# Kernel tuning notes

Hardware: AMD Instinct MI355X
Metric: run time of the kernel (lower is better)

## Reference

```python
import jax, jax.numpy as jnp
import numpy as np

ENS, S_DIM, A_DIM, R_DIM, HID, LAYER_NUM = 7, 30, 8, 1, 200, 5
N_HID_LAYERS = LAYER_NUM - 2  # hidden->hidden Linear+Swish blocks


def swish(x):
    return x * jax.nn.sigmoid(x)


def setup_inputs() -> dict:
    key = jax.random.key(0)
    ks = jax.random.split(key, 14)
    N = 32768
    out_dim = S_DIM + R_DIM
    s = jax.random.normal(ks[0], (N, ENS, S_DIM), dtype=jnp.float32)
    a = jax.random.normal(ks[1], (N, ENS, A_DIM), dtype=jnp.float32)
    sc = 0.05
    W1 = jax.random.normal(ks[2], (ENS, S_DIM + A_DIM, HID), dtype=jnp.float32) * sc
    b1 = jax.random.normal(ks[3], (ENS, HID), dtype=jnp.float32) * sc
    Wh = jax.random.normal(ks[4], (N_HID_LAYERS, ENS, HID, HID), dtype=jnp.float32) * sc
    bh = jax.random.normal(ks[5], (N_HID_LAYERS, ENS, HID), dtype=jnp.float32) * sc
    Wmu = jax.random.normal(ks[6], (ENS, HID, out_dim), dtype=jnp.float32) * sc
    bmu = jax.random.normal(ks[7], (ENS, out_dim), dtype=jnp.float32) * sc
    Wsig = jax.random.normal(ks[8], (ENS, HID, out_dim), dtype=jnp.float32) * sc
    bsig = jax.random.normal(ks[9], (ENS, out_dim), dtype=jnp.float32) * sc
    max_lv_s = jnp.ones((1, S_DIM), dtype=jnp.float32) / 2.0
    min_lv_s = jnp.ones((1, S_DIM), dtype=jnp.float32) * -10.0
    max_lv_r = jnp.ones((1, R_DIM), dtype=jnp.float32) / 2.0
    min_lv_r = jnp.ones((1, R_DIM), dtype=jnp.float32) * -10.0
    return {"s": s, "a": a, "W1": W1, "b1": b1, "Wh": Wh, "bh": bh,
            "Wmu": Wmu, "bmu": bmu, "Wsig": Wsig, "bsig": bsig,
            "max_lv_s": max_lv_s, "min_lv_s": min_lv_s,
            "max_lv_r": max_lv_r, "min_lv_r": min_lv_r}


def reference(s, a, W1, b1, Wh, bh, Wmu, bmu, Wsig, bsig,
              max_lv_s, min_lv_s, max_lv_r, min_lv_r):
    # x: [N, E, s+a]; per-ensemble-member weights batched along E
    x = jnp.concatenate([s, a], axis=-1)
    h = swish(jnp.einsum('ned,edh->neh', x, W1) + b1)
    for i in range(Wh.shape[0]):
        h = swish(jnp.einsum('neh,ehk->nek', h, Wh[i]) + bh[i])
    mu = jnp.einsum('neh,eho->neo', h, Wmu) + bmu      # [N, E, s+r]
    sigma = jnp.einsum('neh,eho->neo', h, Wsig) + bsig  # raw logvar/2
    ds_mu, r_mu = mu[..., :S_DIM], mu[..., S_DIM:]
    ds_sg, r_sg = sigma[..., :S_DIM], sigma[..., S_DIM:]
    # soft clamping of log-variance, then exp
    ds_sg = (max_lv_s - jax.nn.softplus(max_lv_s - 2.0 * ds_sg)) / 2.0
    ds_sg = (min_lv_s + jax.nn.softplus(2.0 * ds_sg - min_lv_s)) / 2.0
    ds_sg = jnp.exp(ds_sg)
    r_sg = (max_lv_r - jax.nn.softplus(max_lv_r - 2.0 * r_sg)) / 2.0
    r_sg = (min_lv_r + jax.nn.softplus(2.0 * r_sg - min_lv_r)) / 2.0
    r_sg = jnp.exp(r_sg)
    return ((ds_mu, ds_sg), (r_mu, r_sg))
```

## Files before the change

kernel.cpp:

```cpp
#include <hip/hip_runtime.h>
#include <hip/hip_bf16.h>

#define ENS 7
#define SDIM 30
#define ADIM 8
#define DIN 38
#define HID 200
#define DOUT 31
#define NHL 3
#define HS 232
#define MT 64

typedef __bf16 bf16x8 __attribute__((ext_vector_type(8)));
typedef float f32x4 __attribute__((ext_vector_type(4)));

#define U_L1 13312
#define U_H 46592
#define OFF_HD2 (U_L1 + NHL * U_H)
#define PER_E (OFF_HD2 + 14336)
#define WS_TOTAL (ENS * PER_E)

__device__ __forceinline__ unsigned short f2bf(float f) {
    unsigned u = __float_as_uint(f);
    u += 0x7fffu + ((u >> 16) & 1u);
    return (unsigned short)(u >> 16);
}

__device__ __forceinline__ unsigned pk2(float a, float b) {
    __hip_bfloat162 h = __float22bfloat162_rn(make_float2(a, b));
    return *reinterpret_cast<unsigned*>(&h);
}

__device__ __forceinline__ float softplusf(float x) {
    return fmaxf(x, 0.f) + __logf(1.f + __expf(-fabsf(x)));
}

__global__ void prep_kernel(const float* __restrict__ W1, const float* __restrict__ Wh,
                            const float* __restrict__ Wmu, const float* __restrict__ Wsig,
                            unsigned short* __restrict__ ws) {
    int idx = blockIdx.x * 256 + threadIdx.x;
    if (idx >= WS_TOTAL) return;
    int e = idx / PER_E, r = idx % PER_E;
    int j = r & 7, lane = (r >> 3) & 63;
    int l16 = lane & 15, q = lane >> 4;
    float v = 0.f;
    if (r < U_L1) {
        int fi = r >> 9;
        int ct = fi >> 1, st = fi & 1;
        int k = st * 32 + q * 8 + j, n = ct * 16 + l16;
        if (k < DIN && n < HID) v = W1[(e * DIN + k) * HID + n];
    } else if (r < OFF_HD2) {
        int rh = r - U_L1;
        int l = rh / U_H, r2 = rh % U_H;
        int fi = r2 >> 9;
        int ct = fi / 7, st = fi % 7;
        int k = st * 32 + q * 8 + j, n = ct * 16 + l16;
        if (k < HID && n < HID) v = Wh[((l * ENS + e) * HID + (long)k) * HID + n];
    } else {
        int r2 = r - OFF_HD2;
        int fi = r2 >> 9;
        int ct = fi / 7, st = fi % 7;
        int k = st * 32 + q * 8 + j, n = ct * 16 + l16;
        if (k < HID) {
            if (n < DOUT) v = Wmu[(e * HID + k) * DOUT + n];
            else if (n >= 32 && n < 32 + DOUT) v = Wsig[(e * HID + k) * DOUT + (n - 32)];
        }
    }
    ws[idx] = f2bf(v);
}

template<int S, int OWN, bool SH>
__device__ __forceinline__ void runLayer(const unsigned short* __restrict__ fo,
                                         const unsigned short* __restrict__ fs,
                                         const unsigned short* hA,
                                         int lo, int swv, int l16, int quad,
                                         f32x4 (&accO)[4][3], f32x4& accS) {
#pragma unroll
    for (int r = 0; r < 4; r++)
#pragma unroll
        for (int c = 0; c < 3; c++) accO[r][c] = (f32x4){0.f, 0.f, 0.f, 0.f};
    accS = (f32x4){0.f, 0.f, 0.f, 0.f};

#pragma unroll
    for (int st = 0; st < S; ++st) {
        bf16x8 bq[4];
#pragma unroll
        for (int c = 0; c < OWN; c++) bq[c] = *((const bf16x8*)(fo + (c * S + st) * 512 + lo));
        if (SH) bq[3] = *((const bf16x8*)(fs + st * 512 + lo));
        bf16x8 af[4];
#pragma unroll
        for (int r = 0; r < 4; r++)
            af[r] = *((const bf16x8*)(hA + (r * 16 + l16) * HS + st * 32 + quad * 8));
        bf16x8 afs;
        if (SH) afs = *((const bf16x8*)(hA + (swv * 16 + l16) * HS + st * 32 + quad * 8));
#pragma unroll
        for (int c = 0; c < OWN; c++)
#pragma unroll
            for (int r = 0; r < 4; r++)
                accO[r][c] = __builtin_amdgcn_mfma_f32_16x16x32_bf16(bq[c], af[r], accO[r][c], 0, 0, 0);
        if (SH) accS = __builtin_amdgcn_mfma_f32_16x16x32_bf16(bq[3], afs, accS, 0, 0, 0);
    }
}

__launch_bounds__(256, 4)
__global__ void ens_mlp_kernel(const float* __restrict__ s, const float* __restrict__ a,
                               const float* __restrict__ b1, const float* __restrict__ bh,
                               const float* __restrict__ bmu, const float* __restrict__ bsig,
                               const float* __restrict__ maxs, const float* __restrict__ mins,
                               const float* __restrict__ maxr, const float* __restrict__ minr,
                               const unsigned short* __restrict__ ws,
                               float* __restrict__ out, int N) {
    __shared__ unsigned short hA[MT * HS];

    const int tid = threadIdx.x;
    const int wv = tid >> 6, lane = tid & 63;
    const int quad = lane >> 4, l16 = lane & 15;
    const int swv = __builtin_amdgcn_readfirstlane(wv);
    const int lo = lane * 8;
    const int bid = blockIdx.x;
    const int e = bid % ENS, n0 = (bid / ENS) * MT;

    for (int i = tid; i < MT * HS / 8; i += 256) ((uint4*)hA)[i] = make_uint4(0, 0, 0, 0);
    __syncthreads();

    {
        int m = tid & 63, cg = tid >> 6;
        long g = n0 + m;
        const float* srow = s + (g * ENS + e) * SDIM;
        const float* arow = a + (g * ENS + e) * ADIM;
#pragma unroll
        for (int k = 0; k < 10; k++) {
            int c = cg * 10 + k;
            if (c < DIN) {
                float v = (c < SDIM) ? srow[c] : arow[c - SDIM];
                hA[m * HS + c] = f2bf(v);
            }
        }
    }
    __syncthreads();

    const unsigned short* we = ws + e * PER_E;
    const unsigned short* L1o = we + swv * 3 * 2 * 512;
    const unsigned short* L1s = we + 12 * 2 * 512;
    const unsigned short* H0o = we + U_L1 + swv * 3 * 7 * 512;
    const unsigned short* H0s = we + U_L1 + 12 * 7 * 512;
    const unsigned short* H1o = H0o + U_H;
    const unsigned short* H1s = H0s + U_H;
    const unsigned short* H2o = H1o + U_H;
    const unsigned short* H2s = H1s + U_H;
    const unsigned short* HDo = we + OFF_HD2 + swv * 7 * 512;

    f32x4 accO[4][3];
    f32x4 accS;

    auto epiH = [&](const float* bias) {
#pragma unroll
        for (int c = 0; c < 3; c++) {
            int col = (3 * swv + c) * 16 + quad * 4;
            float4 bc4 = *((const float4*)(bias + col));
#pragma unroll
            for (int r = 0; r < 4; r++) {
                float v0 = accO[r][c][0] + bc4.x, v1 = accO[r][c][1] + bc4.y;
                float v2 = accO[r][c][2] + bc4.z, v3 = accO[r][c][3] + bc4.w;
                v0 *= __builtin_amdgcn_rcpf(1.f + __expf(-v0));
                v1 *= __builtin_amdgcn_rcpf(1.f + __expf(-v1));
                v2 *= __builtin_amdgcn_rcpf(1.f + __expf(-v2));
                v3 *= __builtin_amdgcn_rcpf(1.f + __expf(-v3));
                *((uint2*)(hA + (r * 16 + l16) * HS + col)) = make_uint2(pk2(v0, v1), pk2(v2, v3));
            }
        }
        {
            int col = 192 + quad * 4;
            float4 bc4 = make_float4(0.f, 0.f, 0.f, 0.f);
            if (col < HID) bc4 = *((const float4*)(bias + col));
            float v0 = accS[0] + bc4.x, v1 = accS[1] + bc4.y;
            float v2 = accS[2] + bc4.z, v3 = accS[3] + bc4.w;
            v0 *= __builtin_amdgcn_rcpf(1.f + __expf(-v0));
            v1 *= __builtin_amdgcn_rcpf(1.f + __expf(-v1));
            v2 *= __builtin_amdgcn_rcpf(1.f + __expf(-v2));
            v3 *= __builtin_amdgcn_rcpf(1.f + __expf(-v3));
            *((uint2*)(hA + (swv * 16 + l16) * HS + col)) = make_uint2(pk2(v0, v1), pk2(v2, v3));
        }
    };

    runLayer<2, 3, true>(L1o, L1s, hA, lo, swv, l16, quad, accO, accS);
    __syncthreads();
    epiH(b1 + e * HID);
    __syncthreads();
    runLayer<7, 3, true>(H0o, H0s, hA, lo, swv, l16, quad, accO, accS);
    __syncthreads();
    epiH(bh + (0 * ENS + e) * HID);
    __syncthreads();
    runLayer<7, 3, true>(H1o, H1s, hA, lo, swv, l16, quad, accO, accS);
    __syncthreads();
    epiH(bh + (1 * ENS + e) * HID);
    __syncthreads();
    runLayer<7, 3, true>(H2o, H2s, hA, lo, swv, l16, quad, accO, accS);
    __syncthreads();
    epiH(bh + (2 * ENS + e) * HID);
    __syncthreads();
    runLayer<7, 1, false>(HDo, (const unsigned short*)nullptr,
                          hA, lo, swv, l16, quad, accO, accS);

    const long off1 = (long)N * ENS * SDIM;
    const long off2 = 2 * off1;
    const long off3 = off2 + (long)N * ENS;
    {
        const bool isSig = (swv >= 2);
        const int c0 = (swv & 1) * 16 + quad * 4;
        float bias_i[4], mx_i[4], mn_i[4];
#pragma unroll
        for (int i = 0; i < 4; i++) {
            int c = c0 + i;
            bias_i[i] = (c < DOUT) ? (isSig ? bsig : bmu)[e * DOUT + c] : 0.f;
            if (isSig) {
                mx_i[i] = (c < SDIM) ? maxs[c] : maxr[0];
                mn_i[i] = (c < SDIM) ? mins[c] : minr[0];
            }
        }
#pragma unroll
        for (int r = 0; r < 4; r++) {
            long g = n0 + r * 16 + l16;
            long rowbase = (g * ENS + e) * SDIM;
#pragma unroll
            for (int i = 0; i < 4; i++) {
                int c = c0 + i;
                if (c < DOUT) {
                    float v = accO[r][0][i] + bias_i[i];
                    if (!isSig) {
                        if (c < SDIM) out[rowbase + c] = v;
                        else out[off2 + g * ENS + e] = v;
                    } else {
                        v = 0.5f * (mx_i[i] - softplusf(mx_i[i] - 2.f * v));
                        v = 0.5f * (mn_i[i] + softplusf(2.f * v - mn_i[i]));
                        v = __expf(v);
                        if (c < SDIM) out[off1 + rowbase + c] = v;
                        else out[off3 + g * ENS + e] = v;
                    }
                }
            }
        }
    }
}

extern "C" void kernel_launch(void* const* d_in, const int* in_sizes, int n_in,
                              void* d_out, int out_size, void* d_ws, size_t ws_size,
                              hipStream_t stream) {
    const float* s    = (const float*)d_in[0];
    const float* a    = (const float*)d_in[1];
    const float* W1   = (const float*)d_in[2];
    const float* b1   = (const float*)d_in[3];
    const float* Wh   = (const float*)d_in[4];
    const float* bh   = (const float*)d_in[5];
    const float* Wmu  = (const float*)d_in[6];
    const float* bmu  = (const float*)d_in[7];
    const float* Wsig = (const float*)d_in[8];
    const float* bsig = (const float*)d_in[9];
    const float* maxs = (const float*)d_in[10];
    const float* mins = (const float*)d_in[11];
    const float* maxr = (const float*)d_in[12];
    const float* minr = (const float*)d_in[13];
    float* out = (float*)d_out;
    unsigned short* ws = (unsigned short*)d_ws;

    int N = in_sizes[0] / (ENS * SDIM);

    int prepBlocks = (WS_TOTAL + 255) / 256;
    prep_kernel<<<prepBlocks, 256, 0, stream>>>(W1, Wh, Wmu, Wsig, ws);

    int mainBlocks = (N / MT) * ENS;
    ens_mlp_kernel<<<mainBlocks, 256, 0, stream>>>(s, a, b1, bh, bmu, bsig,
                                                   maxs, mins, maxr, minr, ws, out, N);
}
```

Baseline: 264.7 us.

## Double-buffer weight fragment loads across k-steps and layers, ensemble-major block order

```diff
diff --git a/kernel.cpp b/kernel.cpp
--- a/kernel.cpp
+++ b/kernel.cpp
@@ -69,24 +69,31 @@
     ws[idx] = f2bf(v);
 }
 
-template<int S, int OWN, bool SH>
+template<int S, int OWN, bool SH, int NS, int NOWN, bool NSH>
 __device__ __forceinline__ void runLayer(const unsigned short* __restrict__ fo,
                                          const unsigned short* __restrict__ fs,
+                                         const unsigned short* __restrict__ nfo,
+                                         const unsigned short* __restrict__ nfs,
                                          const unsigned short* hA,
                                          int lo, int swv, int l16, int quad,
-                                         f32x4 (&accO)[4][3], f32x4& accS) {
+                                         f32x4 (&accO)[4][3], f32x4& accS,
+                                         bf16x8 (&bq)[4], bf16x8 (&bt)[4]) {
 #pragma unroll
     for (int r = 0; r < 4; r++)
 #pragma unroll
         for (int c = 0; c < 3; c++) accO[r][c] = (f32x4){0.f, 0.f, 0.f, 0.f};
     accS = (f32x4){0.f, 0.f, 0.f, 0.f};
 
-#pragma unroll
-    for (int st = 0; st < S; ++st) {
-        bf16x8 bq[4];
-#pragma unroll
-        for (int c = 0; c < OWN; c++) bq[c] = *((const bf16x8*)(fo + (c * S + st) * 512 + lo));
-        if (SH) bq[3] = *((const bf16x8*)(fs + st * 512 + lo));
+    auto body = [&](bf16x8 (&cur)[4], bf16x8 (&nxt)[4], int st) {
+        if (st + 1 < S) {
+#pragma unroll
+            for (int c = 0; c < OWN; c++) nxt[c] = *((const bf16x8*)(fo + (c * S + st + 1) * 512 + lo));
+            if (SH) nxt[3] = *((const bf16x8*)(fs + (st + 1) * 512 + lo));
+        } else if (NS > 0) {
+#pragma unroll
+            for (int c = 0; c < NOWN; c++) nxt[c] = *((const bf16x8*)(nfo + (c * NS) * 512 + lo));
+            if (NSH) nxt[3] = *((const bf16x8*)(nfs + lo));
+        }
         bf16x8 af[4];
 #pragma unroll
         for (int r = 0; r < 4; r++)
@@ -97,12 +104,18 @@
         for (int c = 0; c < OWN; c++)
 #pragma unroll
             for (int r = 0; r < 4; r++)
-                accO[r][c] = __builtin_amdgcn_mfma_f32_16x16x32_bf16(bq[c], af[r], accO[r][c], 0, 0, 0);
-        if (SH) accS = __builtin_amdgcn_mfma_f32_16x16x32_bf16(bq[3], afs, accS, 0, 0, 0);
-    }
-}
-
-__launch_bounds__(256, 4)
+                accO[r][c] = __builtin_amdgcn_mfma_f32_16x16x32_bf16(cur[c], af[r], accO[r][c], 0, 0, 0);
+        if (SH) accS = __builtin_amdgcn_mfma_f32_16x16x32_bf16(cur[3], afs, accS, 0, 0, 0);
+    };
+
+#pragma unroll
+    for (int st = 0; st < S; ++st) {
+        if ((st & 1) == 0) body(bq, bt, st);
+        else               body(bt, bq, st);
+    }
+}
+
+__launch_bounds__(256, 3)
 __global__ void ens_mlp_kernel(const float* __restrict__ s, const float* __restrict__ a,
                                const float* __restrict__ b1, const float* __restrict__ bh,
                                const float* __restrict__ bmu, const float* __restrict__ bsig,
@@ -118,10 +131,17 @@
     const int swv = __builtin_amdgcn_readfirstlane(wv);
     const int lo = lane * 8;
     const int bid = blockIdx.x;
-    const int e = bid % ENS, n0 = (bid / ENS) * MT;
-
-    for (int i = tid; i < MT * HS / 8; i += 256) ((uint4*)hA)[i] = make_uint4(0, 0, 0, 0);
-    __syncthreads();
+    const int bpe = N / MT;
+    const int e = bid / bpe, n0 = (bid - e * bpe) * MT;
+
+    for (int t = tid; t < MT * 13; t += 256) {
+        int row = t / 13, k = t - row * 13;
+        *((unsigned*)(hA + row * HS + 38 + 2 * k)) = 0u;
+    }
+    for (int t = tid; t < MT * 12; t += 256) {
+        int row = t / 12, k = t - row * 12;
+        *((unsigned*)(hA + row * HS + 208 + 2 * k)) = 0u;
+    }
 
     {
         int m = tid & 63, cg = tid >> 6;
@@ -152,6 +172,7 @@
 
     f32x4 accO[4][3];
     f32x4 accS;
+    bf16x8 bqA[4], bqB[4];
 
     auto epiH = [&](const float* bias) {
 #pragma unroll
@@ -183,24 +204,30 @@
         }
     };
 
-    runLayer<2, 3, true>(L1o, L1s, hA, lo, swv, l16, quad, accO, accS);
+#pragma unroll
+    for (int c = 0; c < 3; c++) bqA[c] = *((const bf16x8*)(L1o + (c * 2) * 512 + lo));
+    bqA[3] = *((const bf16x8*)(L1s + lo));
+
+    runLayer<2, 3, true, 7, 3, true>(L1o, L1s, H0o, H0s, hA, lo, swv, l16, quad, accO, accS, bqA, bqB);
     __syncthreads();
     epiH(b1 + e * HID);
     __syncthreads();
-    runLayer<7, 3, true>(H0o, H0s, hA, lo, swv, l16, quad, accO, accS);
+    runLayer<7, 3, true, 7, 3, true>(H0o, H0s, H1o, H1s, hA, lo, swv, l16, quad, accO, accS, bqA, bqB);
     __syncthreads();
     epiH(bh + (0 * ENS + e) * HID);
     __syncthreads();
-    runLayer<7, 3, true>(H1o, H1s, hA, lo, swv, l16, quad, accO, accS);
+    runLayer<7, 3, true, 7, 3, true>(H1o, H1s, H2o, H2s, hA, lo, swv, l16, quad, accO, accS, bqB, bqA);
     __syncthreads();
     epiH(bh + (1 * ENS + e) * HID);
     __syncthreads();
-    runLayer<7, 3, true>(H2o, H2s, hA, lo, swv, l16, quad, accO, accS);
+    runLayer<7, 3, true, 7, 1, false>(H2o, H2s, HDo, (const unsigned short*)nullptr,
+                                      hA, lo, swv, l16, quad, accO, accS, bqA, bqB);
     __syncthreads();
     epiH(bh + (2 * ENS + e) * HID);
     __syncthreads();
-    runLayer<7, 1, false>(HDo, (const unsigned short*)nullptr,
-                          hA, lo, swv, l16, quad, accO, accS);
+    runLayer<7, 1, false, 0, 0, false>(HDo, (const unsigned short*)nullptr,
+                                       (const unsigned short*)nullptr, (const unsigned short*)nullptr,
+                                       hA, lo, swv, l16, quad, accO, accS, bqB, bqA);
 
     const long off1 = (long)N * ENS * SDIM;
     const long off2 = 2 * off1;
```

New measurement: 252.0 us. 4.8% less time.

## Give each wave its own 16 rows across all columns to drop block barriers

Applied to the files above, without the earlier changes.

```diff
diff --git a/kernel.cpp b/kernel.cpp
--- a/kernel.cpp
+++ b/kernel.cpp
@@ -69,40 +69,25 @@
     ws[idx] = f2bf(v);
 }
 
-template<int S, int OWN, bool SH>
-__device__ __forceinline__ void runLayer(const unsigned short* __restrict__ fo,
-                                         const unsigned short* __restrict__ fs,
-                                         const unsigned short* hA,
-                                         int lo, int swv, int l16, int quad,
-                                         f32x4 (&accO)[4][3], f32x4& accS) {
-#pragma unroll
-    for (int r = 0; r < 4; r++)
-#pragma unroll
-        for (int c = 0; c < 3; c++) accO[r][c] = (f32x4){0.f, 0.f, 0.f, 0.f};
-    accS = (f32x4){0.f, 0.f, 0.f, 0.f};
-
+template<int S, int NCT>
+__device__ __forceinline__ void runLayerW(const unsigned short* __restrict__ wbase,
+                                          const unsigned short* hrow,
+                                          int lo, int quad,
+                                          f32x4* acc) {
 #pragma unroll
     for (int st = 0; st < S; ++st) {
-        bf16x8 bq[4];
-#pragma unroll
-        for (int c = 0; c < OWN; c++) bq[c] = *((const bf16x8*)(fo + (c * S + st) * 512 + lo));
-        if (SH) bq[3] = *((const bf16x8*)(fs + st * 512 + lo));
-        bf16x8 af[4];
-#pragma unroll
-        for (int r = 0; r < 4; r++)
-            af[r] = *((const bf16x8*)(hA + (r * 16 + l16) * HS + st * 32 + quad * 8));
-        bf16x8 afs;
-        if (SH) afs = *((const bf16x8*)(hA + (swv * 16 + l16) * HS + st * 32 + quad * 8));
-#pragma unroll
-        for (int c = 0; c < OWN; c++)
-#pragma unroll
-            for (int r = 0; r < 4; r++)
-                accO[r][c] = __builtin_amdgcn_mfma_f32_16x16x32_bf16(bq[c], af[r], accO[r][c], 0, 0, 0);
-        if (SH) accS = __builtin_amdgcn_mfma_f32_16x16x32_bf16(bq[3], afs, accS, 0, 0, 0);
-    }
-}
-
-__launch_bounds__(256, 4)
+        bf16x8 af = *((const bf16x8*)(hrow + st * 32 + quad * 8));
+        bf16x8 bq[NCT];
+#pragma unroll
+        for (int ct = 0; ct < NCT; ct++)
+            bq[ct] = *((const bf16x8*)(wbase + (ct * S + st) * 512 + lo));
+#pragma unroll
+        for (int ct = 0; ct < NCT; ct++)
+            acc[ct] = __builtin_amdgcn_mfma_f32_16x16x32_bf16(bq[ct], af, acc[ct], 0, 0, 0);
+    }
+}
+
+__launch_bounds__(256, 3)
 __global__ void ens_mlp_kernel(const float* __restrict__ s, const float* __restrict__ a,
                                const float* __restrict__ b1, const float* __restrict__ bh,
                                const float* __restrict__ bmu, const float* __restrict__ bsig,
@@ -113,130 +98,115 @@
     __shared__ unsigned short hA[MT * HS];
 
     const int tid = threadIdx.x;
-    const int wv = tid >> 6, lane = tid & 63;
+    const int lane = tid & 63;
     const int quad = lane >> 4, l16 = lane & 15;
-    const int swv = __builtin_amdgcn_readfirstlane(wv);
+    const int swv = __builtin_amdgcn_readfirstlane(tid >> 6);
     const int lo = lane * 8;
     const int bid = blockIdx.x;
-    const int e = bid % ENS, n0 = (bid / ENS) * MT;
-
-    for (int i = tid; i < MT * HS / 8; i += 256) ((uint4*)hA)[i] = make_uint4(0, 0, 0, 0);
-    __syncthreads();
+    const int bpe = N / MT;
+    const int e = bid / bpe, n0 = (bid - e * bpe) * MT;
+
+    const int row = swv * 16 + l16;
+    const long g = n0 + row;
+    unsigned short* hrow = hA + row * HS;
 
     {
-        int m = tid & 63, cg = tid >> 6;
-        long g = n0 + m;
         const float* srow = s + (g * ENS + e) * SDIM;
         const float* arow = a + (g * ENS + e) * ADIM;
 #pragma unroll
-        for (int k = 0; k < 10; k++) {
-            int c = cg * 10 + k;
-            if (c < DIN) {
-                float v = (c < SDIM) ? srow[c] : arow[c - SDIM];
-                hA[m * HS + c] = f2bf(v);
+        for (int i = 0; i < 5; i++) {
+            int idx = quad + 4 * i;
+            if (idx < 19) {
+                float2 p = (idx < 15) ? *((const float2*)(srow + 2 * idx))
+                                      : *((const float2*)(arow + 2 * (idx - 15)));
+                *((unsigned*)(hrow + 2 * idx)) = pk2(p.x, p.y);
             }
         }
-    }
-    __syncthreads();
+#pragma unroll
+        for (int i = 0; i < 4; i++) {
+            int k = quad + 4 * i;
+            if (k < 13) *((unsigned*)(hrow + 38 + 2 * k)) = 0u;
+            if (k < 12) *((unsigned*)(hrow + 208 + 2 * k)) = 0u;
+        }
+    }
 
     const unsigned short* we = ws + e * PER_E;
-    const unsigned short* L1o = we + swv * 3 * 2 * 512;
-    const unsigned short* L1s = we + 12 * 2 * 512;
-    const unsigned short* H0o = we + U_L1 + swv * 3 * 7 * 512;
-    const unsigned short* H0s = we + U_L1 + 12 * 7 * 512;
-    const unsigned short* H1o = H0o + U_H;
-    const unsigned short* H1s = H0s + U_H;
-    const unsigned short* H2o = H1o + U_H;
-    const unsigned short* H2s = H1s + U_H;
-    const unsigned short* HDo = we + OFF_HD2 + swv * 7 * 512;
-
-    f32x4 accO[4][3];
-    f32x4 accS;
-
-    auto epiH = [&](const float* bias) {
-#pragma unroll
-        for (int c = 0; c < 3; c++) {
-            int col = (3 * swv + c) * 16 + quad * 4;
-            float4 bc4 = *((const float4*)(bias + col));
-#pragma unroll
-            for (int r = 0; r < 4; r++) {
-                float v0 = accO[r][c][0] + bc4.x, v1 = accO[r][c][1] + bc4.y;
-                float v2 = accO[r][c][2] + bc4.z, v3 = accO[r][c][3] + bc4.w;
-                v0 *= __builtin_amdgcn_rcpf(1.f + __expf(-v0));
-                v1 *= __builtin_amdgcn_rcpf(1.f + __expf(-v1));
-                v2 *= __builtin_amdgcn_rcpf(1.f + __expf(-v2));
-                v3 *= __builtin_amdgcn_rcpf(1.f + __expf(-v3));
-                *((uint2*)(hA + (r * 16 + l16) * HS + col)) = make_uint2(pk2(v0, v1), pk2(v2, v3));
-            }
-        }
-        {
-            int col = 192 + quad * 4;
-            float4 bc4 = make_float4(0.f, 0.f, 0.f, 0.f);
-            if (col < HID) bc4 = *((const float4*)(bias + col));
-            float v0 = accS[0] + bc4.x, v1 = accS[1] + bc4.y;
-            float v2 = accS[2] + bc4.z, v3 = accS[3] + bc4.w;
+
+    f32x4 acc[13];
+
+    auto loadBias = [&](const float* bias) {
+#pragma unroll
+        for (int ct = 0; ct < 12; ct++)
+            *((float4*)&acc[ct]) = *((const float4*)(bias + ct * 16 + quad * 4));
+        acc[12] = (f32x4){0.f, 0.f, 0.f, 0.f};
+        if (quad < 2) *((float4*)&acc[12]) = *((const float4*)(bias + 192 + quad * 4));
+    };
+
+    auto epi = [&]() {
+#pragma unroll
+        for (int ct = 0; ct < 13; ct++) {
+            int col = ct * 16 + quad * 4;
+            float v0 = acc[ct][0], v1 = acc[ct][1];
+            float v2 = acc[ct][2], v3 = acc[ct][3];
             v0 *= __builtin_amdgcn_rcpf(1.f + __expf(-v0));
             v1 *= __builtin_amdgcn_rcpf(1.f + __expf(-v1));
             v2 *= __builtin_amdgcn_rcpf(1.f + __expf(-v2));
             v3 *= __builtin_amdgcn_rcpf(1.f + __expf(-v3));
-            *((uint2*)(hA + (swv * 16 + l16) * HS + col)) = make_uint2(pk2(v0, v1), pk2(v2, v3));
+            *((uint2*)(hrow + col)) = make_uint2(pk2(v0, v1), pk2(v2, v3));
         }
     };
 
-    runLayer<2, 3, true>(L1o, L1s, hA, lo, swv, l16, quad, accO, accS);
-    __syncthreads();
-    epiH(b1 + e * HID);
-    __syncthreads();
-    runLayer<7, 3, true>(H0o, H0s, hA, lo, swv, l16, quad, accO, accS);
-    __syncthreads();
-    epiH(bh + (0 * ENS + e) * HID);
-    __syncthreads();
-    runLayer<7, 3, true>(H1o, H1s, hA, lo, swv, l16, quad, accO, accS);
-    __syncthreads();
-    epiH(bh + (1 * ENS + e) * HID);
-    __syncthreads();
-    runLayer<7, 3, true>(H2o, H2s, hA, lo, swv, l16, quad, accO, accS);
-    __syncthreads();
-    epiH(bh + (2 * ENS + e) * HID);
-    __syncthreads();
-    runLayer<7, 1, false>(HDo, (const unsigned short*)nullptr,
-                          hA, lo, swv, l16, quad, accO, accS);
+    loadBias(b1 + e * HID);
+    runLayerW<2, 13>(we, hrow, lo, quad, acc);
+    epi();
+    loadBias(bh + (0 * ENS + e) * HID);
+    runLayerW<7, 13>(we + U_L1 + 0 * U_H, hrow, lo, quad, acc);
+    epi();
+    loadBias(bh + (1 * ENS + e) * HID);
+    runLayerW<7, 13>(we + U_L1 + 1 * U_H, hrow, lo, quad, acc);
+    epi();
+    loadBias(bh + (2 * ENS + e) * HID);
+    runLayerW<7, 13>(we + U_L1 + 2 * U_H, hrow, lo, quad, acc);
+    epi();
+
+    {
+#pragma unroll
+        for (int ct = 0; ct < 4; ct++) {
+            const float* hb = (ct >= 2) ? bsig : bmu;
+            f32x4 iH = (f32x4){0.f, 0.f, 0.f, 0.f};
+#pragma unroll
+            for (int i = 0; i < 4; i++) {
+                int c = (ct & 1) * 16 + quad * 4 + i;
+                if (c < DOUT) iH[i] = hb[e * DOUT + c];
+            }
+            acc[ct] = iH;
+        }
+    }
+    runLayerW<7, 4>(we + OFF_HD2, hrow, lo, quad, acc);
 
     const long off1 = (long)N * ENS * SDIM;
     const long off2 = 2 * off1;
     const long off3 = off2 + (long)N * ENS;
-    {
-        const bool isSig = (swv >= 2);
-        const int c0 = (swv & 1) * 16 + quad * 4;
-        float bias_i[4], mx_i[4], mn_i[4];
+    const long rowbase = (g * ENS + e) * SDIM;
+#pragma unroll
+    for (int ct = 0; ct < 4; ct++) {
+        const bool isSig = (ct >= 2);
 #pragma unroll
         for (int i = 0; i < 4; i++) {
-            int c = c0 + i;
-            bias_i[i] = (c < DOUT) ? (isSig ? bsig : bmu)[e * DOUT + c] : 0.f;
-            if (isSig) {
-                mx_i[i] = (c < SDIM) ? maxs[c] : maxr[0];
-                mn_i[i] = (c < SDIM) ? mins[c] : minr[0];
-            }
-        }
-#pragma unroll
-        for (int r = 0; r < 4; r++) {
-            long g = n0 + r * 16 + l16;
-            long rowbase = (g * ENS + e) * SDIM;
-#pragma unroll
-            for (int i = 0; i < 4; i++) {
-                int c = c0 + i;
-                if (c < DOUT) {
-                    float v = accO[r][0][i] + bias_i[i];
-                    if (!isSig) {
-                        if (c < SDIM) out[rowbase + c] = v;
-                        else out[off2 + g * ENS + e] = v;
-                    } else {
-                        v = 0.5f * (mx_i[i] - softplusf(mx_i[i] - 2.f * v));
-                        v = 0.5f * (mn_i[i] + softplusf(2.f * v - mn_i[i]));
-                        v = __expf(v);
-                        if (c < SDIM) out[off1 + rowbase + c] = v;
-                        else out[off3 + g * ENS + e] = v;
-                    }
+            int c = (ct & 1) * 16 + quad * 4 + i;
+            if (c < DOUT) {
+                float v = acc[ct][i];
+                if (!isSig) {
+                    if (c < SDIM) out[rowbase + c] = v;
+                    else out[off2 + g * ENS + e] = v;
+                } else {
+                    float mx = (c < SDIM) ? maxs[c] : maxr[0];
+                    float mn = (c < SDIM) ? mins[c] : minr[0];
+                    v = 0.5f * (mx - softplusf(mx - 2.f * v));
+                    v = 0.5f * (mn + softplusf(2.f * v - mn));
+                    v = __expf(v);
+                    if (c < SDIM) out[off1 + rowbase + c] = v;
+                    else out[off3 + g * ENS + e] = v;
                 }
             }
         }
```

Result: slower. 290.4 us (+9.7%).
